# Kernel optimization log

Hardware: AMD Instinct MI355X
Metric: run time of the kernel (lower is better)

## Reference

```python
import math
import jax, jax.numpy as jnp
import numpy as np

B, T, C = 2, 768, 64
N_HEAD = 64
HEAD_DIM = C // N_HEAD  # = 1 (forced by the Kronecker-lift shape constraint)


def _alibi_slopes(n_heads):
    def pow2_slopes(n):
        start = 2 ** (-2 ** (-(math.log2(n) - 3)))
        return [start * (start ** i) for i in range(n)]
    if math.log2(n_heads).is_integer():
        s = pow2_slopes(n_heads)
    else:
        closest = 2 ** math.floor(math.log2(n_heads))
        s = pow2_slopes(closest)
        s.extend(pow2_slopes(2 * closest)[0::2][: n_heads - closest])
    return np.asarray(s, dtype=np.float32)


def _kron_block_apply(z, tmp):
    """Apply M.T where M = block_diag_h(kron(eye(hd), tmp[h])). z:(B,T,C), tmp:(H,hd,hd).
    Per head-block, for z reshaped (a,d) over (hd,hd): out[a,c] = sum_d tmp[h,c,d] * z[a,d]."""
    Bz, Tz, Cz = z.shape
    H, hd, _ = tmp.shape
    zr = z.reshape(Bz, Tz, H, hd, hd)
    return jnp.einsum('bthad,hcd->bthac', zr, tmp).reshape(Bz, Tz, Cz)


def setup_inputs() -> dict:
    key = jax.random.key(0)
    kx, kw, kv, kp = jax.random.split(key, 4)
    x = jax.random.normal(kx, (B, T, C), dtype=jnp.float32)
    W_attn = jax.random.normal(kw, (2 * C, C), dtype=jnp.float32) * 0.02
    v_tmp = jax.random.normal(kv, (N_HEAD, HEAD_DIM, HEAD_DIM), dtype=jnp.float32)
    proj_tmp = jax.random.normal(kp, (N_HEAD, HEAD_DIM, HEAD_DIM), dtype=jnp.float32)
    return {"x": x, "W_attn": W_attn, "v_tmp": v_tmp, "proj_tmp": proj_tmp}


def reference(x, W_attn, v_tmp, proj_tmp):
    Bx, Tx, Cx = x.shape
    H = v_tmp.shape[0]
    head_dim = Cx // H
    # q, k projection (use_v=True -> c_attn maps C -> 2C, no bias)
    qk = x @ W_attn.T
    q, k = jnp.split(qk, 2, axis=-1)
    # Kronecker-lifted V transform (block-diagonal structure applied directly)
    v = _kron_block_apply(x, v_tmp)
    # (B,T,H,d) -> (B,H,T,d)
    q = q.reshape(Bx, Tx, H, head_dim).transpose(0, 2, 1, 3)
    k = k.reshape(Bx, Tx, H, head_dim).transpose(0, 2, 1, 3)
    v = v.reshape(Bx, Tx, H, head_dim).transpose(0, 2, 1, 3)
    scale = 1.0 / math.sqrt(head_dim)
    scores = jnp.einsum('bhid,bhjd->bhij', q, k) * scale
    # ALiBi bias: positions clamped at 0 (NOTE: source has no causal -inf mask)
    pos = jnp.minimum(jnp.arange(Tx)[None, :] - jnp.arange(Tx)[:, None], 0).astype(x.dtype)
    slopes = jnp.asarray(_alibi_slopes(H), dtype=x.dtype)
    scores = scores + slopes[None, :, None, None] * pos[None, None, :, :]
    w = jax.nn.softmax(scores, axis=-1)
    y = jnp.einsum('bhij,bhjd->bhid', w, v)
    y = y.transpose(0, 2, 1, 3).reshape(Bx, Tx, Cx)
    # Kronecker-lifted output projection
    y = _kron_block_apply(y, proj_tmp)
    return y
```

## Files before the change

kernel.cpp:

```cpp
#include <hip/hip_runtime.h>
#include <stdint.h>

constexpr int Tc = 768;
constexpr int Hc = 64;
constexpr int Bc = 2;
constexpr int NT = 12;
constexpr float LOG2E = 1.44269504088896f;
constexpr float LN2   = 0.69314718056f;
constexpr size_t SLAB = (size_t)Bc * Hc * Tc;

typedef float v2f __attribute__((ext_vector_type(2)));
typedef float v4f __attribute__((ext_vector_type(4)));

__device__ __forceinline__ float dpp_reduce_add(float v) {
    v += __int_as_float(__builtin_amdgcn_update_dpp(0, __float_as_int(v), 0x111, 0xf, 0xf, true));
    v += __int_as_float(__builtin_amdgcn_update_dpp(0, __float_as_int(v), 0x112, 0xf, 0xf, true));
    v += __int_as_float(__builtin_amdgcn_update_dpp(0, __float_as_int(v), 0x114, 0xf, 0xf, true));
    v += __int_as_float(__builtin_amdgcn_update_dpp(0, __float_as_int(v), 0x118, 0xf, 0xf, true));
    v += __int_as_float(__builtin_amdgcn_update_dpp(0, __float_as_int(v), 0x142, 0xf, 0xf, true));
    v += __int_as_float(__builtin_amdgcn_update_dpp(0, __float_as_int(v), 0x143, 0xf, 0xf, true));
    return v;
}

__global__ __launch_bounds__(64) void proj_mom_kernel(
    const float* __restrict__ x, const float* __restrict__ W,
    const float* __restrict__ vtmp, const float* __restrict__ ptmp,
    float* __restrict__ qs, float* __restrict__ ks, float* __restrict__ vs,
    float* __restrict__ MOM)
{
    const int lane = threadIdx.x & 63;
    const int bx   = blockIdx.x;
    const int b    = bx / NT;
    const int B    = bx - b * NT;
    const int t    = B * 64 + lane;
    const int g    = bx * 64 + lane;
    const int h    = blockIdx.y;
    const int bh   = b * Hc + h;

    const v4f* xp = (const v4f*)(x + (size_t)g * 64);
    const float* __restrict__ wq = W + h * 64;
    const float* __restrict__ wk = W + (64 + h) * 64;
    float aq = 0.f, ak = 0.f;
#pragma unroll
    for (int c = 0; c < 16; ++c) {
        v4f u = xp[c];
        aq = fmaf(u.x, wq[4*c],   aq);  ak = fmaf(u.x, wk[4*c],   ak);
        aq = fmaf(u.y, wq[4*c+1], aq);  ak = fmaf(u.y, wk[4*c+1], ak);
        aq = fmaf(u.z, wq[4*c+2], aq);  ak = fmaf(u.z, wk[4*c+2], ak);
        aq = fmaf(u.w, wq[4*c+3], aq);  ak = fmaf(u.w, wk[4*c+3], ak);
    }
    const float vv = x[(size_t)g * 64 + h] * vtmp[h] * ptmp[h];
    const size_t o = (size_t)bh * Tc + t;
    qs[o] = aq * LOG2E;
    ks[o] = ak;
    vs[o] = vv;

    const float slope2 = exp2f(-0.125f * (float)(h + 1)) * LOG2E;
    const float lf = exp2f(slope2 * (float)(lane - 63));

    float km[8];
    km[0] = 1.f;
#pragma unroll
    for (int m = 1; m < 8; ++m) km[m] = km[m - 1] * ak;

    float r[32];
#pragma unroll
    for (int m = 0; m < 8; ++m) {
        const float kl2 = km[m] * lf;
        r[m]      = km[m];
        r[8 + m]  = km[m] * vv;
        r[16 + m] = kl2;
        r[24 + m] = kl2 * vv;
    }
#define DPP_PASS(CTRL)                                                        \
    _Pragma("unroll")                                                         \
    for (int ii = 0; ii < 32; ++ii)                                           \
        r[ii] += __int_as_float(__builtin_amdgcn_update_dpp(                  \
            0, __float_as_int(r[ii]), CTRL, 0xf, 0xf, true));
    DPP_PASS(0x111)
    DPP_PASS(0x112)
    DPP_PASS(0x114)
    DPP_PASS(0x118)
    DPP_PASS(0x142)
    DPP_PASS(0x143)
#undef DPP_PASS

    if (lane == 63) {
        float* mp = MOM + ((size_t)bh * NT + B) * 32;
#pragma unroll
        for (int m = 0; m < 8; ++m) {
            v4f s4 = { r[4*m], r[4*m+1], r[4*m+2], r[4*m+3] };
            *(v4f*)(mp + 4 * m) = s4;
        }
    }
}

__global__ __launch_bounds__(256, 6) void attn_kernel(
    const float* __restrict__ qs, const float* __restrict__ ks,
    const float* __restrict__ vs, const float* __restrict__ MOM,
    float* __restrict__ out)
{
    const int tid  = threadIdx.x;
    const int lane = tid & 63;
    const int w    = __builtin_amdgcn_readfirstlane(tid >> 6);
    const int rt   = blockIdx.x;
    const int h    = blockIdx.y;
    const int b    = blockIdx.z;
    const int bh   = b * Hc + h;

    __shared__ float kd[64], vd[64];
    __shared__ float psum[4][64], pacc[4][64];

    if (tid < 64)       kd[tid]      = ks[(size_t)bh * Tc + rt * 64 + tid];
    else if (tid < 128) vd[tid - 64] = vs[(size_t)bh * Tc + rt * 64 + tid - 64];

    const int i = rt * 64 + lane;
    const float q2 = qs[(size_t)bh * Tc + i];
    const float slope2 = exp2f(-0.125f * (float)(h + 1)) * LOG2E;
    const float fi2 = slope2 * (float)i;

    const float z  = q2 * LN2;
    const float p1 = z;
    const float p2 = z * p1 * 0.5f;
    const float p3 = z * p2 * (1.f / 3.f);
    const float p4 = z * p3 * 0.25f;
    const float p5 = z * p4 * 0.2f;
    const float p6 = z * p5 * (1.f / 6.f);
    const float p7 = z * p6 * (1.f / 7.f);

    float S = 0.f, A = 0.f;

    for (int B = w; B < NT; B += 4) {
        if (B == rt) continue;
        const float* __restrict__ mp = MOM + ((size_t)bh * NT + B) * 32;
        if (B > rt) {
            float s0 = mp[0], a0 = mp[8];
            s0 = fmaf(p1, mp[1], s0);  a0 = fmaf(p1, mp[9],  a0);
            s0 = fmaf(p2, mp[2], s0);  a0 = fmaf(p2, mp[10], a0);
            s0 = fmaf(p3, mp[3], s0);  a0 = fmaf(p3, mp[11], a0);
            s0 = fmaf(p4, mp[4], s0);  a0 = fmaf(p4, mp[12], a0);
            s0 = fmaf(p5, mp[5], s0);  a0 = fmaf(p5, mp[13], a0);
            s0 = fmaf(p6, mp[6], s0);  a0 = fmaf(p6, mp[14], a0);
            s0 = fmaf(p7, mp[7], s0);  a0 = fmaf(p7, mp[15], a0);
            S += s0;  A += a0;
        } else {
            const float f = exp2f(slope2 * (float)(B * 64 + 63) - fi2);
            float s0 = mp[16], a0 = mp[24];
            s0 = fmaf(p1, mp[17], s0); a0 = fmaf(p1, mp[25], a0);
            s0 = fmaf(p2, mp[18], s0); a0 = fmaf(p2, mp[26], a0);
            s0 = fmaf(p3, mp[19], s0); a0 = fmaf(p3, mp[27], a0);
            s0 = fmaf(p4, mp[20], s0); a0 = fmaf(p4, mp[28], a0);
            s0 = fmaf(p5, mp[21], s0); a0 = fmaf(p5, mp[29], a0);
            s0 = fmaf(p6, mp[22], s0); a0 = fmaf(p6, mp[30], a0);
            s0 = fmaf(p7, mp[23], s0); a0 = fmaf(p7, mp[31], a0);
            S = fmaf(f, s0, S);  A = fmaf(f, a0, A);
        }
    }

    __syncthreads();

    v2f cu2[8];
#pragma unroll
    for (int u = 0; u < 8; ++u) {
        cu2[u].x = slope2 * (float)(2 * u);
        cu2[u].y = slope2 * (float)(2 * u + 1);
    }
    const float mb = slope2 * (float)(rt * 64 + 16 * w) - fi2;
    const v2f mb2 = {mb, mb};
    const v2f q2v = {q2, q2};
    v2f sum2 = {0.f, 0.f}, acc2 = {0.f, 0.f};
    const v2f* __restrict__ k2p = (const v2f*)kd;
    const v2f* __restrict__ v2p = (const v2f*)vd;
#pragma unroll
    for (int u = 0; u < 8; ++u) {
        v2f k2 = k2p[8 * w + u];
        v2f v2 = v2p[8 * w + u];
        v2f t2 = mb2 + cu2[u];
        v2f bias;
        bias.x = fminf(t2.x, 0.f);
        bias.y = fminf(t2.y, 0.f);
        v2f sc = q2v * k2 + bias;
        v2f e;
        e.x = __builtin_amdgcn_exp2f(sc.x);
        e.y = __builtin_amdgcn_exp2f(sc.y);
        sum2 += e;
        acc2 = e * v2 + acc2;
    }
    S += sum2.x + sum2.y;
    A += acc2.x + acc2.y;

    psum[w][lane] = S;
    pacc[w][lane] = A;
    __syncthreads();

    if (tid < 64) {
        float s = psum[0][lane] + psum[1][lane] + psum[2][lane] + psum[3][lane];
        float a = pacc[0][lane] + pacc[1][lane] + pacc[2][lane] + pacc[3][lane];
        out[((size_t)(b * Tc + rt * 64 + lane)) * 64 + h] =
            a * __builtin_amdgcn_rcpf(s);
    }
}

extern "C" void kernel_launch(void* const* d_in, const int* in_sizes, int n_in,
                              void* d_out, int out_size, void* d_ws, size_t ws_size,
                              hipStream_t stream) {
    const float* x    = (const float*)d_in[0];
    const float* W    = (const float*)d_in[1];
    const float* vtmp = (const float*)d_in[2];
    const float* ptmp = (const float*)d_in[3];
    float* out = (float*)d_out;

    float* qsl = (float*)d_ws;
    float* ksl = qsl + SLAB;
    float* vsl = ksl + SLAB;
    float* mom = vsl + SLAB;

    proj_mom_kernel<<<dim3(24, Hc), 64, 0, stream>>>(
        x, W, vtmp, ptmp, qsl, ksl, vsl, mom);
    attn_kernel<<<dim3(NT, Hc, Bc), 256, 0, stream>>>(
        qsl, ksl, vsl, mom, out);
}
```

Measured before the change: 68.92 us.

## Pre-combine per-block moments in shared memory before per-row polynomial evaluation

The attention kernel now stages all of a head's block moments in LDS. Before any per-row work, 32 threads sum the future-block moments and the decay-weighted past-block moments. Each row then evaluates a single degree-7 polynomial for each side, with one exp2 factor for the past side, instead of looping over up to 12 blocks with per-block exp2 and global loads. This cuts redundant per-row work and global memory traffic. The cost is an extra barrier and a short serial reduction over blocks.

```diff
diff --git a/kernel.cpp b/kernel.cpp
--- a/kernel.cpp
+++ b/kernel.cpp
@@ -11,16 +11,6 @@
 
 typedef float v2f __attribute__((ext_vector_type(2)));
 typedef float v4f __attribute__((ext_vector_type(4)));
-
-__device__ __forceinline__ float dpp_reduce_add(float v) {
-    v += __int_as_float(__builtin_amdgcn_update_dpp(0, __float_as_int(v), 0x111, 0xf, 0xf, true));
-    v += __int_as_float(__builtin_amdgcn_update_dpp(0, __float_as_int(v), 0x112, 0xf, 0xf, true));
-    v += __int_as_float(__builtin_amdgcn_update_dpp(0, __float_as_int(v), 0x114, 0xf, 0xf, true));
-    v += __int_as_float(__builtin_amdgcn_update_dpp(0, __float_as_int(v), 0x118, 0xf, 0xf, true));
-    v += __int_as_float(__builtin_amdgcn_update_dpp(0, __float_as_int(v), 0x142, 0xf, 0xf, true));
-    v += __int_as_float(__builtin_amdgcn_update_dpp(0, __float_as_int(v), 0x143, 0xf, 0xf, true));
-    return v;
-}
 
 __global__ __launch_bounds__(64) void proj_mom_kernel(
     const float* __restrict__ x, const float* __restrict__ W,
@@ -108,15 +98,44 @@
     const int b    = blockIdx.z;
     const int bh   = b * Hc + h;
 
+    __shared__ float momL[NT * 32];
     __shared__ float kd[64], vd[64];
+    __shared__ float comb[32];
     __shared__ float psum[4][64], pacc[4][64];
 
-    if (tid < 64)       kd[tid]      = ks[(size_t)bh * Tc + rt * 64 + tid];
-    else if (tid < 128) vd[tid - 64] = vs[(size_t)bh * Tc + rt * 64 + tid - 64];
+    {
+        const float* __restrict__ mbp = MOM + (size_t)bh * (NT * 32);
+        if (tid < 128) {
+            momL[tid]       = mbp[tid];
+            momL[tid + 128] = mbp[tid + 128];
+            momL[tid + 256] = mbp[tid + 256];
+        } else if (tid < 192) {
+            kd[tid - 128] = ks[(size_t)bh * Tc + rt * 64 + (tid - 128)];
+        } else {
+            vd[tid - 192] = vs[(size_t)bh * Tc + rt * 64 + (tid - 192)];
+        }
+    }
+    const float slope2 = exp2f(-0.125f * (float)(h + 1)) * LOG2E;
+    __syncthreads();
+
+    if (tid < 32) {
+        const int grp = tid >> 4;
+        const int m16 = tid & 15;
+        float acc = 0.f;
+        if (grp == 0) {
+            for (int B = rt + 1; B < NT; ++B)
+                acc += momL[B * 32 + m16];
+        } else {
+            for (int B = 0; B < rt; ++B)
+                acc = fmaf(exp2f(slope2 * (float)(64 * (B - rt) + 63)),
+                           momL[B * 32 + 16 + m16], acc);
+        }
+        comb[tid] = acc;
+    }
+    __syncthreads();
 
     const int i = rt * 64 + lane;
     const float q2 = qs[(size_t)bh * Tc + i];
-    const float slope2 = exp2f(-0.125f * (float)(h + 1)) * LOG2E;
     const float fi2 = slope2 * (float)i;
 
     const float z  = q2 * LN2;
@@ -129,35 +148,31 @@
     const float p7 = z * p6 * (1.f / 7.f);
 
     float S = 0.f, A = 0.f;
-
-    for (int B = w; B < NT; B += 4) {
-        if (B == rt) continue;
-        const float* __restrict__ mp = MOM + ((size_t)bh * NT + B) * 32;
-        if (B > rt) {
-            float s0 = mp[0], a0 = mp[8];
-            s0 = fmaf(p1, mp[1], s0);  a0 = fmaf(p1, mp[9],  a0);
-            s0 = fmaf(p2, mp[2], s0);  a0 = fmaf(p2, mp[10], a0);
-            s0 = fmaf(p3, mp[3], s0);  a0 = fmaf(p3, mp[11], a0);
-            s0 = fmaf(p4, mp[4], s0);  a0 = fmaf(p4, mp[12], a0);
-            s0 = fmaf(p5, mp[5], s0);  a0 = fmaf(p5, mp[13], a0);
-            s0 = fmaf(p6, mp[6], s0);  a0 = fmaf(p6, mp[14], a0);
-            s0 = fmaf(p7, mp[7], s0);  a0 = fmaf(p7, mp[15], a0);
-            S += s0;  A += a0;
-        } else {
-            const float f = exp2f(slope2 * (float)(B * 64 + 63) - fi2);
-            float s0 = mp[16], a0 = mp[24];
-            s0 = fmaf(p1, mp[17], s0); a0 = fmaf(p1, mp[25], a0);
-            s0 = fmaf(p2, mp[18], s0); a0 = fmaf(p2, mp[26], a0);
-            s0 = fmaf(p3, mp[19], s0); a0 = fmaf(p3, mp[27], a0);
-            s0 = fmaf(p4, mp[20], s0); a0 = fmaf(p4, mp[28], a0);
-            s0 = fmaf(p5, mp[21], s0); a0 = fmaf(p5, mp[29], a0);
-            s0 = fmaf(p6, mp[22], s0); a0 = fmaf(p6, mp[30], a0);
-            s0 = fmaf(p7, mp[23], s0); a0 = fmaf(p7, mp[31], a0);
-            S = fmaf(f, s0, S);  A = fmaf(f, a0, A);
-        }
-    }
-
-    __syncthreads();
+    if (w == 0) {
+        float sf = comb[0];
+        sf = fmaf(p1, comb[1], sf); sf = fmaf(p2, comb[2], sf);
+        sf = fmaf(p3, comb[3], sf); sf = fmaf(p4, comb[4], sf);
+        sf = fmaf(p5, comb[5], sf); sf = fmaf(p6, comb[6], sf);
+        sf = fmaf(p7, comb[7], sf);
+        float af = comb[8];
+        af = fmaf(p1, comb[9],  af); af = fmaf(p2, comb[10], af);
+        af = fmaf(p3, comb[11], af); af = fmaf(p4, comb[12], af);
+        af = fmaf(p5, comb[13], af); af = fmaf(p6, comb[14], af);
+        af = fmaf(p7, comb[15], af);
+        float sp = comb[16];
+        sp = fmaf(p1, comb[17], sp); sp = fmaf(p2, comb[18], sp);
+        sp = fmaf(p3, comb[19], sp); sp = fmaf(p4, comb[20], sp);
+        sp = fmaf(p5, comb[21], sp); sp = fmaf(p6, comb[22], sp);
+        sp = fmaf(p7, comb[23], sp);
+        float ap = comb[24];
+        ap = fmaf(p1, comb[25], ap); ap = fmaf(p2, comb[26], ap);
+        ap = fmaf(p3, comb[27], ap); ap = fmaf(p4, comb[28], ap);
+        ap = fmaf(p5, comb[29], ap); ap = fmaf(p6, comb[30], ap);
+        ap = fmaf(p7, comb[31], ap);
+        const float f = __builtin_amdgcn_exp2f(-slope2 * (float)lane);
+        S = fmaf(f, sp, sf);
+        A = fmaf(f, ap, af);
+    }
 
     v2f cu2[8];
 #pragma unroll
```

Measured after the change: 67.27 us. -2.4%, faster.
